# Kernel tuning notes

Measured on AMD Instinct MI355X. Metric: run time of the kernel, lower is better.

The kernel has to match this reference:

```python
import jax, jax.numpy as jnp
import numpy as np

THRESH = 0.7
MIN_KEPT_FRAC = 0.5  # max(0.001, 0.5)
LOG_CLAMP = -100.0   # torch BCELoss clamps log terms at -100


def setup_inputs() -> dict:
    key = jax.random.key(0)
    k1, k2 = jax.random.split(key)
    shape = (32, 1, 1024, 1024)
    pred = jax.random.uniform(k1, shape, dtype=jnp.float32, minval=1e-6, maxval=1.0 - 1e-6)
    target = jnp.round(jax.random.uniform(k2, shape, dtype=jnp.float32))  # binary mask
    return {"pred": pred, "target": target}


def reference(pred, target):
    p = pred.reshape(-1)
    t = target.reshape(-1)
    # elementwise BCE with reduction='none' (torch clamps log at -100)
    log_p = jnp.clip(jnp.log(p), LOG_CLAMP, None)
    log_1mp = jnp.clip(jnp.log1p(-p), LOG_CLAMP, None)
    pixel_losses = -(t * log_p + (1.0 - t) * log_1mp)

    n = p.shape[0]
    min_kept = min(int(MIN_KEPT_FRAC * (n - 1)), n - 1)  # static python int
    p_sorted = jnp.sort(p)
    min_value = p_sorted[min_kept]
    threshold = jnp.maximum(min_value, jnp.float32(THRESH))

    # keeping losses whose pred value is below the threshold; mean over kept
    mask = p < threshold
    cnt = jnp.sum(mask).astype(pixel_losses.dtype)
    return jnp.sum(jnp.where(mask, pixel_losses, 0.0)) / cnt
```

## Files before the change

### kernel.cpp

```cpp
#include <hip/hip_runtime.h>

#define THRESH   0.7f
#define BASEU    0x3F333334u
#define NBINS    2048
#define NSUB     4096
#define NTHREADS 256
#define IPT4     4
#define NITER    4
#define F4_PER_BLOCK (NTHREADS * IPT4 * NITER)
#define MAXBLK   8192
#define NBLK_FB  1024

struct Blk { float sum_lt, sum_eq; unsigned cnt_lt, cnt_eq; };

struct Ws {
  Blk      blk[MAXBLK];
  double   sum_lt, sum_eq;
  double   prefix_sum;
  unsigned cnt_lt, cnt_eq;
  unsigned done;
  unsigned fin3, fin5;
  unsigned selBin, rank_r, prefix_cnt;
  unsigned Hcnt[NBINS];
  float    Hsum[NBINS];
  unsigned subCnt[NSUB];
  float    subSum[NSUB];
};

__device__ __forceinline__ float bce_loss(float p, float t) {
  float x = (t > 0.5f) ? p : (1.0f - p);
  return -fmaxf(__logf(x), -100.0f);
}

__global__ __launch_bounds__(NTHREADS) void k_main(
    const float4* __restrict__ p4, const float4* __restrict__ t4,
    Ws* __restrict__ ws, int n) {
  const int nvec = n >> 2;
  const int start = blockIdx.x * F4_PER_BLOCK;

  float s_lt = 0.f, s_eq = 0.f;
  unsigned c_lt = 0u, c_eq = 0u;

  if (start + F4_PER_BLOCK <= nvec) {
    for (int it = 0; it < NITER; ++it) {
      const int base = start + it * (NTHREADS * IPT4) + threadIdx.x;
      float4 pr[IPT4], tr[IPT4];
#pragma unroll
      for (int j = 0; j < IPT4; ++j) pr[j] = p4[base + j * NTHREADS];
#pragma unroll
      for (int j = 0; j < IPT4; ++j) tr[j] = t4[base + j * NTHREADS];
#pragma unroll
      for (int j = 0; j < IPT4; ++j) {
        float pa[4] = {pr[j].x, pr[j].y, pr[j].z, pr[j].w};
        float ta[4] = {tr[j].x, tr[j].y, tr[j].z, tr[j].w};
#pragma unroll
        for (int c = 0; c < 4; ++c) {
          float pv = pa[c];
          float loss = bce_loss(pv, ta[c]);
          if (pv < THRESH)       { c_lt++; s_lt += loss; }
          else if (pv == THRESH) { c_eq++; s_eq += loss; }
        }
      }
    }
  } else {
    for (int it = 0; it < NITER; ++it) {
      const int base = start + it * (NTHREADS * IPT4) + threadIdx.x;
#pragma unroll
      for (int j = 0; j < IPT4; ++j) {
        int id = base + j * NTHREADS;
        if (id < nvec) {
          float4 p = p4[id];
          float4 t = t4[id];
          float pa[4] = {p.x, p.y, p.z, p.w};
          float ta[4] = {t.x, t.y, t.z, t.w};
#pragma unroll
          for (int c = 0; c < 4; ++c) {
            float pv = pa[c];
            float loss = bce_loss(pv, ta[c]);
            if (pv < THRESH)       { c_lt++; s_lt += loss; }
            else if (pv == THRESH) { c_eq++; s_eq += loss; }
          }
        }
      }
    }
    int i = (nvec << 2) + threadIdx.x;
    if (blockIdx.x == gridDim.x - 1 && i < n) {
      float pv = ((const float*)p4)[i];
      float loss = bce_loss(pv, ((const float*)t4)[i]);
      if (pv < THRESH)       { c_lt++; s_lt += loss; }
      else if (pv == THRESH) { c_eq++; s_eq += loss; }
    }
  }

#pragma unroll
  for (int off = 32; off > 0; off >>= 1) {
    s_lt += __shfl_down(s_lt, off);
    s_eq += __shfl_down(s_eq, off);
    c_lt += __shfl_down(c_lt, off);
    c_eq += __shfl_down(c_eq, off);
  }
  __shared__ float    red_slt[4], red_seq[4];
  __shared__ unsigned red_clt[4], red_ceq[4];
  int wave = threadIdx.x >> 6;
  if ((threadIdx.x & 63) == 0) {
    red_slt[wave] = s_lt; red_seq[wave] = s_eq;
    red_clt[wave] = c_lt; red_ceq[wave] = c_eq;
  }
  __syncthreads();
  if (threadIdx.x == 0) {
    Blk b;
    b.sum_lt = red_slt[0] + red_slt[1] + red_slt[2] + red_slt[3];
    b.sum_eq = red_seq[0] + red_seq[1] + red_seq[2] + red_seq[3];
    b.cnt_lt = red_clt[0] + red_clt[1] + red_clt[2] + red_clt[3];
    b.cnt_eq = red_ceq[0] + red_ceq[1] + red_ceq[2] + red_ceq[3];
    ws->blk[blockIdx.x] = b;
  }
}

__global__ __launch_bounds__(1024) void k_reduce(
    float* __restrict__ out, Ws* __restrict__ ws, int nblk, int kidx) {
  double s_lt = 0.0, s_eq = 0.0;
  unsigned long long c_lt = 0, c_eq = 0;
  for (int i = threadIdx.x; i < nblk; i += 1024) {
    Blk b = ws->blk[i];
    s_lt += (double)b.sum_lt; s_eq += (double)b.sum_eq;
    c_lt += b.cnt_lt;         c_eq += b.cnt_eq;
  }
#pragma unroll
  for (int off = 32; off > 0; off >>= 1) {
    s_lt += __shfl_down(s_lt, off);
    s_eq += __shfl_down(s_eq, off);
    c_lt += __shfl_down(c_lt, off);
    c_eq += __shfl_down(c_eq, off);
  }
  __shared__ double    rs[16], rq[16];
  __shared__ unsigned long long rc[16], re[16];
  int wave = threadIdx.x >> 6;
  if ((threadIdx.x & 63) == 0) { rs[wave] = s_lt; rq[wave] = s_eq; rc[wave] = c_lt; re[wave] = c_eq; }
  __syncthreads();
  if (threadIdx.x == 0) {
    double slt = 0.0, seq = 0.0; unsigned long long clt = 0, ceq = 0;
    for (int w = 0; w < 16; ++w) { slt += rs[w]; seq += rq[w]; clt += rc[w]; ceq += re[w]; }
    ws->sum_lt = slt; ws->sum_eq = seq;
    ws->cnt_lt = (unsigned)clt; ws->cnt_eq = (unsigned)ceq;
    if (clt + ceq > (unsigned long long)kidx) {
      out[0] = (float)(slt / (double)clt);
      ws->done = 1u;
    }
  }
}

__global__ __launch_bounds__(NTHREADS) void k_hist(
    const float* __restrict__ pred, const float* __restrict__ targ,
    Ws* __restrict__ ws, int n, int kidx, int nblocks) {
  if (ws->done) return;
  __shared__ unsigned hc[NBINS];
  __shared__ float    hs[NBINS];
  for (int i = threadIdx.x; i < NBINS; i += NTHREADS) { hc[i] = 0u; hs[i] = 0.f; }
  __syncthreads();

  int tid = blockIdx.x * blockDim.x + threadIdx.x;
  int stride = gridDim.x * blockDim.x;
  int nvec = n >> 2;
  const float4* p4 = (const float4*)pred;
  const float4* t4 = (const float4*)targ;
  for (int i = tid; i < nvec; i += stride) {
    float4 p = p4[i];
    float4 t = t4[i];
    float pa[4] = {p.x, p.y, p.z, p.w};
    float ta[4] = {t.x, t.y, t.z, t.w};
#pragma unroll
    for (int c = 0; c < 4; ++c) {
      float pv = pa[c];
      if (pv > THRESH) {
        unsigned b = (__float_as_uint(pv) - BASEU) >> 12;
        if (b > NBINS - 1) b = NBINS - 1;
        atomicAdd(&hc[b], 1u);
        atomicAdd(&hs[b], bce_loss(pv, ta[c]));
      }
    }
  }
  for (int i = (nvec << 2) + tid; i < n; i += stride) {
    float pv = pred[i];
    if (pv > THRESH) {
      unsigned b = (__float_as_uint(pv) - BASEU) >> 12;
      if (b > NBINS - 1) b = NBINS - 1;
      atomicAdd(&hc[b], 1u);
      atomicAdd(&hs[b], bce_loss(pv, targ[i]));
    }
  }
  __syncthreads();
  for (int i = threadIdx.x; i < NBINS; i += NTHREADS) {
    if (hc[i])        atomicAdd(&ws->Hcnt[i], hc[i]);
    if (hs[i] != 0.f) atomicAdd(&ws->Hsum[i], hs[i]);
  }
  __threadfence();
  if (threadIdx.x == 0) {
    unsigned prev = atomicAdd(&ws->fin3, 1u);
    if (prev == (unsigned)(nblocks - 1)) {
      __threadfence();
      unsigned long long cum  = (unsigned long long)ws->cnt_lt + ws->cnt_eq;
      double             csum = ws->sum_lt + ws->sum_eq;
      for (int b = 0; b < NBINS; ++b) {
        unsigned hcnt = atomicAdd(&ws->Hcnt[b], 0u);
        if (cum + hcnt > (unsigned long long)kidx) {
          ws->selBin     = (unsigned)b;
          ws->rank_r     = (unsigned)((unsigned long long)kidx - cum);
          ws->prefix_cnt = (unsigned)cum;
          ws->prefix_sum = csum;
          break;
        }
        cum  += hcnt;
        csum += (double)atomicAdd(&ws->Hsum[b], 0.f);
      }
    }
  }
}

__global__ __launch_bounds__(NTHREADS) void k_sub(
    const float* __restrict__ pred, const float* __restrict__ targ,
    float* __restrict__ out, Ws* __restrict__ ws, int n, int nblocks) {
  if (ws->done) return;
  unsigned base = BASEU + (ws->selBin << 12);
  __shared__ unsigned sc[NSUB];
  __shared__ float    ssm[NSUB];
  for (int i = threadIdx.x; i < NSUB; i += NTHREADS) { sc[i] = 0u; ssm[i] = 0.f; }
  __syncthreads();

  int tid = blockIdx.x * blockDim.x + threadIdx.x;
  int stride = gridDim.x * blockDim.x;
  int nvec = n >> 2;
  const float4* p4 = (const float4*)pred;
  const float4* t4 = (const float4*)targ;
  for (int i = tid; i < nvec; i += stride) {
    float4 p = p4[i];
    float4 t = t4[i];
    float pa[4] = {p.x, p.y, p.z, p.w};
    float ta[4] = {t.x, t.y, t.z, t.w};
#pragma unroll
    for (int c = 0; c < 4; ++c) {
      unsigned u = __float_as_uint(pa[c]);
      if (u >= base && u < base + NSUB) {
        atomicAdd(&sc[u - base], 1u);
        atomicAdd(&ssm[u - base], bce_loss(pa[c], ta[c]));
      }
    }
  }
  for (int i = (nvec << 2) + tid; i < n; i += stride) {
    unsigned u = __float_as_uint(pred[i]);
    if (u >= base && u < base + NSUB) {
      atomicAdd(&sc[u - base], 1u);
      atomicAdd(&ssm[u - base], bce_loss(pred[i], targ[i]));
    }
  }
  __syncthreads();
  for (int i = threadIdx.x; i < NSUB; i += NTHREADS) {
    if (sc[i])         atomicAdd(&ws->subCnt[i], sc[i]);
    if (ssm[i] != 0.f) atomicAdd(&ws->subSum[i], ssm[i]);
  }
  __threadfence();
  if (threadIdx.x == 0) {
    unsigned prev = atomicAdd(&ws->fin5, 1u);
    if (prev == (unsigned)(nblocks - 1)) {
      __threadfence();
      unsigned r = ws->rank_r;
      unsigned long long cum = 0;
      double csum = 0.0;
      for (int i = 0; i < NSUB; ++i) {
        unsigned c = atomicAdd(&ws->subCnt[i], 0u);
        if (cum + c > (unsigned long long)r) {
          unsigned long long cnt_final = (unsigned long long)ws->prefix_cnt + cum;
          double sum_final = ws->prefix_sum + csum;
          out[0] = (float)(sum_final / (double)cnt_final);
          break;
        }
        cum  += c;
        csum += (double)atomicAdd(&ws->subSum[i], 0.f);
      }
    }
  }
}

extern "C" void kernel_launch(void* const* d_in, const int* in_sizes, int n_in,
                              void* d_out, int out_size, void* d_ws, size_t ws_size,
                              hipStream_t stream) {
  const float* pred = (const float*)d_in[0];
  const float* targ = (const float*)d_in[1];
  float* out = (float*)d_out;
  Ws* ws = (Ws*)d_ws;
  int n = in_sizes[0];
  long long kll = (long long)(n - 1) / 2;
  if (kll > (long long)(n - 1)) kll = n - 1;
  int kidx = (int)kll;

  int nvec = n >> 2;
  int nblk = (nvec + F4_PER_BLOCK - 1) / F4_PER_BLOCK;
  if (nblk < 1) nblk = 1;
  if (nblk > MAXBLK) nblk = MAXBLK;

  hipMemsetAsync(d_ws, 0, sizeof(Ws), stream);
  k_main  <<<nblk, NTHREADS, 0, stream>>>((const float4*)pred, (const float4*)targ, ws, n);
  k_reduce<<<1, 1024, 0, stream>>>(out, ws, nblk, kidx);
  k_hist  <<<NBLK_FB, NTHREADS, 0, stream>>>(pred, targ, ws, n, kidx, NBLK_FB);
  k_sub   <<<NBLK_FB, NTHREADS, 0, stream>>>(pred, targ, out, ws, n, NBLK_FB);
}
```

Baseline: 290.7 us.

## Drop workspace memset, merge fallback kernels with grid sync, software-pipeline main loads

Removes the full-workspace hipMemsetAsync and resets counters inside the decide kernel instead. The two fallback histogram kernels become one kernel that clears its own arrays and uses spin-based grid barriers. The main pass gains a grid-stride chunk loop with double-buffered float4 loads, branchless lt accumulation with a wave-level __any guard for the equality case, and launch bounds requesting 4 blocks per CU. This cuts launch and memset overhead and improves memory-level parallelism, but the spin barrier risks deadlock if all 1024 fallback blocks are not co-resident.

```diff
diff --git a/kernel.cpp b/kernel.cpp
--- a/kernel.cpp
+++ b/kernel.cpp
@@ -5,9 +5,7 @@
 #define NBINS    2048
 #define NSUB     4096
 #define NTHREADS 256
-#define IPT4     4
-#define NITER    4
-#define F4_PER_BLOCK (NTHREADS * IPT4 * NITER)
+#define F4_PER_CHUNK 4096
 #define MAXBLK   8192
 #define NBLK_FB  1024
 
@@ -15,11 +13,10 @@
 
 struct Ws {
   Blk      blk[MAXBLK];
-  double   sum_lt, sum_eq;
-  double   prefix_sum;
+  double   sum_lt, sum_eq, prefix_sum;
   unsigned cnt_lt, cnt_eq;
   unsigned done;
-  unsigned fin3, fin5;
+  unsigned fin0, fin1, fin2, fin3;
   unsigned selBin, rank_r, prefix_cnt;
   unsigned Hcnt[NBINS];
   float    Hsum[NBINS];
@@ -29,66 +26,80 @@
 
 __device__ __forceinline__ float bce_loss(float p, float t) {
   float x = (t > 0.5f) ? p : (1.0f - p);
-  return -fmaxf(__logf(x), -100.0f);
-}
-
-__global__ __launch_bounds__(NTHREADS) void k_main(
+  return fminf(-__logf(x), 100.0f);
+}
+
+__global__ __launch_bounds__(NTHREADS, 4) void k_main(
     const float4* __restrict__ p4, const float4* __restrict__ t4,
-    Ws* __restrict__ ws, int n) {
+    Ws* __restrict__ ws, int n, int nchunks) {
   const int nvec = n >> 2;
-  const int start = blockIdx.x * F4_PER_BLOCK;
-
   float s_lt = 0.f, s_eq = 0.f;
   unsigned c_lt = 0u, c_eq = 0u;
 
-  if (start + F4_PER_BLOCK <= nvec) {
-    for (int it = 0; it < NITER; ++it) {
-      const int base = start + it * (NTHREADS * IPT4) + threadIdx.x;
-      float4 pr[IPT4], tr[IPT4];
-#pragma unroll
-      for (int j = 0; j < IPT4; ++j) pr[j] = p4[base + j * NTHREADS];
-#pragma unroll
-      for (int j = 0; j < IPT4; ++j) tr[j] = t4[base + j * NTHREADS];
-#pragma unroll
-      for (int j = 0; j < IPT4; ++j) {
-        float pa[4] = {pr[j].x, pr[j].y, pr[j].z, pr[j].w};
-        float ta[4] = {tr[j].x, tr[j].y, tr[j].z, tr[j].w};
+#define CONSUME(PR, TR)                                                        \
+  _Pragma("unroll") for (int j = 0; j < 4; ++j) {                              \
+    float pa[4] = {PR[j].x, PR[j].y, PR[j].z, PR[j].w};                        \
+    float ta[4] = {TR[j].x, TR[j].y, TR[j].z, TR[j].w};                        \
+    _Pragma("unroll") for (int c = 0; c < 4; ++c) {                            \
+      float pv = pa[c];                                                        \
+      float x  = (ta[c] > 0.5f) ? pv : (1.0f - pv);                            \
+      float l  = fminf(-__logf(x), 100.0f);                                    \
+      bool lt  = (pv < THRESH);                                                \
+      s_lt += lt ? l : 0.0f;                                                   \
+      c_lt += lt ? 1u : 0u;                                                    \
+      if (__any(pv == THRESH)) {               \
+        bool eq = (pv == THRESH);                                              \
+        c_eq += eq ? 1u : 0u;                                                  \
+        s_eq += eq ? l : 0.0f;                                                 \
+      }                                                                        \
+    }                                                                          \
+  }
+#define LOADB(PR, TR, IT)                                                      \
+  _Pragma("unroll") for (int j = 0; j < 4; ++j) {                              \
+    PR[j] = pp[(IT) * 1024 + j * 256];                                         \
+    TR[j] = tt[(IT) * 1024 + j * 256];                                         \
+  }
+
+  for (int chunk = blockIdx.x; chunk < nchunks; chunk += gridDim.x) {
+    const int start = chunk * F4_PER_CHUNK;
+    if (start + F4_PER_CHUNK <= nvec) {
+      const float4* pp = p4 + start + threadIdx.x;
+      const float4* tt = t4 + start + threadIdx.x;
+      float4 pA[4], tA[4], pB[4], tB[4];
+      LOADB(pA, tA, 0)
+      LOADB(pB, tB, 1)
+      CONSUME(pA, tA)
+      LOADB(pA, tA, 2)
+      CONSUME(pB, tB)
+      LOADB(pB, tB, 3)
+      CONSUME(pA, tA)
+      CONSUME(pB, tB)
+    } else {
+      int lim = start + F4_PER_CHUNK; if (lim > nvec) lim = nvec;
+      for (int f = start + threadIdx.x; f < lim; f += NTHREADS) {
+        float4 p = p4[f];
+        float4 t = t4[f];
+        float pa[4] = {p.x, p.y, p.z, p.w};
+        float ta[4] = {t.x, t.y, t.z, t.w};
 #pragma unroll
         for (int c = 0; c < 4; ++c) {
           float pv = pa[c];
-          float loss = bce_loss(pv, ta[c]);
-          if (pv < THRESH)       { c_lt++; s_lt += loss; }
-          else if (pv == THRESH) { c_eq++; s_eq += loss; }
+          float l = bce_loss(pv, ta[c]);
+          if (pv < THRESH)       { c_lt++; s_lt += l; }
+          else if (pv == THRESH) { c_eq++; s_eq += l; }
         }
       }
     }
-  } else {
-    for (int it = 0; it < NITER; ++it) {
-      const int base = start + it * (NTHREADS * IPT4) + threadIdx.x;
-#pragma unroll
-      for (int j = 0; j < IPT4; ++j) {
-        int id = base + j * NTHREADS;
-        if (id < nvec) {
-          float4 p = p4[id];
-          float4 t = t4[id];
-          float pa[4] = {p.x, p.y, p.z, p.w};
-          float ta[4] = {t.x, t.y, t.z, t.w};
-#pragma unroll
-          for (int c = 0; c < 4; ++c) {
-            float pv = pa[c];
-            float loss = bce_loss(pv, ta[c]);
-            if (pv < THRESH)       { c_lt++; s_lt += loss; }
-            else if (pv == THRESH) { c_eq++; s_eq += loss; }
-          }
-        }
-      }
-    }
+  }
+#undef LOADB
+#undef CONSUME
+  if (blockIdx.x == 0) {
     int i = (nvec << 2) + threadIdx.x;
-    if (blockIdx.x == gridDim.x - 1 && i < n) {
+    if (i < n) {
       float pv = ((const float*)p4)[i];
-      float loss = bce_loss(pv, ((const float*)t4)[i]);
-      if (pv < THRESH)       { c_lt++; s_lt += loss; }
-      else if (pv == THRESH) { c_eq++; s_eq += loss; }
+      float l = bce_loss(pv, ((const float*)t4)[i]);
+      if (pv < THRESH)       { c_lt++; s_lt += l; }
+      else if (pv == THRESH) { c_eq++; s_eq += l; }
     }
   }
 
@@ -117,7 +128,7 @@
   }
 }
 
-__global__ __launch_bounds__(1024) void k_reduce(
+__global__ __launch_bounds__(1024) void k_decide(
     float* __restrict__ out, Ws* __restrict__ ws, int nblk, int kidx) {
   double s_lt = 0.0, s_eq = 0.0;
   unsigned long long c_lt = 0, c_eq = 0;
@@ -133,7 +144,7 @@
     c_lt += __shfl_down(c_lt, off);
     c_eq += __shfl_down(c_eq, off);
   }
-  __shared__ double    rs[16], rq[16];
+  __shared__ double rs[16], rq[16];
   __shared__ unsigned long long rc[16], re[16];
   int wave = threadIdx.x >> 6;
   if ((threadIdx.x & 63) == 0) { rs[wave] = s_lt; rq[wave] = s_eq; rc[wave] = c_lt; re[wave] = c_eq; }
@@ -143,140 +154,111 @@
     for (int w = 0; w < 16; ++w) { slt += rs[w]; seq += rq[w]; clt += rc[w]; ceq += re[w]; }
     ws->sum_lt = slt; ws->sum_eq = seq;
     ws->cnt_lt = (unsigned)clt; ws->cnt_eq = (unsigned)ceq;
+    ws->fin0 = 0u; ws->fin1 = 0u; ws->fin2 = 0u; ws->fin3 = 0u;
     if (clt + ceq > (unsigned long long)kidx) {
       out[0] = (float)(slt / (double)clt);
       ws->done = 1u;
-    }
-  }
-}
-
-__global__ __launch_bounds__(NTHREADS) void k_hist(
+    } else {
+      ws->done = 0u;
+    }
+  }
+}
+
+__device__ void gsync(unsigned* ctr, unsigned goal) {
+  __syncthreads();
+  if (threadIdx.x == 0) {
+    __threadfence();
+    atomicAdd(ctr, 1u);
+    while (atomicAdd(ctr, 0u) < goal) __builtin_amdgcn_s_sleep(8);
+  }
+  __syncthreads();
+  __threadfence();
+}
+
+__global__ __launch_bounds__(NTHREADS) void k_fallback(
     const float* __restrict__ pred, const float* __restrict__ targ,
-    Ws* __restrict__ ws, int n, int kidx, int nblocks) {
+    float* __restrict__ out, Ws* __restrict__ ws, int n, int kidx) {
   if (ws->done) return;
-  __shared__ unsigned hc[NBINS];
-  __shared__ float    hs[NBINS];
-  for (int i = threadIdx.x; i < NBINS; i += NTHREADS) { hc[i] = 0u; hs[i] = 0.f; }
-  __syncthreads();
-
-  int tid = blockIdx.x * blockDim.x + threadIdx.x;
-  int stride = gridDim.x * blockDim.x;
-  int nvec = n >> 2;
-  const float4* p4 = (const float4*)pred;
-  const float4* t4 = (const float4*)targ;
-  for (int i = tid; i < nvec; i += stride) {
-    float4 p = p4[i];
-    float4 t = t4[i];
-    float pa[4] = {p.x, p.y, p.z, p.w};
-    float ta[4] = {t.x, t.y, t.z, t.w};
-#pragma unroll
-    for (int c = 0; c < 4; ++c) {
-      float pv = pa[c];
-      if (pv > THRESH) {
-        unsigned b = (__float_as_uint(pv) - BASEU) >> 12;
-        if (b > NBINS - 1) b = NBINS - 1;
-        atomicAdd(&hc[b], 1u);
-        atomicAdd(&hs[b], bce_loss(pv, ta[c]));
-      }
-    }
-  }
-  for (int i = (nvec << 2) + tid; i < n; i += stride) {
+
+  __shared__ union {
+    struct { unsigned hc[NBINS]; float hs[NBINS]; } l1;
+    struct { unsigned sc[NSUB];  float ss[NSUB];  } l2;
+  } sh;
+
+  const int gtid = blockIdx.x * NTHREADS + threadIdx.x;
+  const int gstride = gridDim.x * NTHREADS;
+
+  for (int i = gtid; i < NBINS; i += gstride) { ws->Hcnt[i] = 0u; ws->Hsum[i] = 0.f; }
+  for (int i = gtid; i < NSUB;  i += gstride) { ws->subCnt[i] = 0u; ws->subSum[i] = 0.f; }
+  gsync(&ws->fin0, gridDim.x);
+
+  for (int i = threadIdx.x; i < NBINS; i += NTHREADS) { sh.l1.hc[i] = 0u; sh.l1.hs[i] = 0.f; }
+  __syncthreads();
+  for (int i = gtid; i < n; i += gstride) {
     float pv = pred[i];
     if (pv > THRESH) {
       unsigned b = (__float_as_uint(pv) - BASEU) >> 12;
       if (b > NBINS - 1) b = NBINS - 1;
-      atomicAdd(&hc[b], 1u);
-      atomicAdd(&hs[b], bce_loss(pv, targ[i]));
+      atomicAdd(&sh.l1.hc[b], 1u);
+      atomicAdd(&sh.l1.hs[b], bce_loss(pv, targ[i]));
     }
   }
   __syncthreads();
   for (int i = threadIdx.x; i < NBINS; i += NTHREADS) {
-    if (hc[i])        atomicAdd(&ws->Hcnt[i], hc[i]);
-    if (hs[i] != 0.f) atomicAdd(&ws->Hsum[i], hs[i]);
-  }
-  __threadfence();
-  if (threadIdx.x == 0) {
-    unsigned prev = atomicAdd(&ws->fin3, 1u);
-    if (prev == (unsigned)(nblocks - 1)) {
-      __threadfence();
-      unsigned long long cum  = (unsigned long long)ws->cnt_lt + ws->cnt_eq;
-      double             csum = ws->sum_lt + ws->sum_eq;
-      for (int b = 0; b < NBINS; ++b) {
-        unsigned hcnt = atomicAdd(&ws->Hcnt[b], 0u);
-        if (cum + hcnt > (unsigned long long)kidx) {
-          ws->selBin     = (unsigned)b;
-          ws->rank_r     = (unsigned)((unsigned long long)kidx - cum);
-          ws->prefix_cnt = (unsigned)cum;
-          ws->prefix_sum = csum;
-          break;
-        }
-        cum  += hcnt;
-        csum += (double)atomicAdd(&ws->Hsum[b], 0.f);
+    if (sh.l1.hc[i])        atomicAdd(&ws->Hcnt[i], sh.l1.hc[i]);
+    if (sh.l1.hs[i] != 0.f) atomicAdd(&ws->Hsum[i], sh.l1.hs[i]);
+  }
+  gsync(&ws->fin1, gridDim.x);
+
+  if (blockIdx.x == 0 && threadIdx.x == 0) {
+    unsigned long long cum = (unsigned long long)ws->cnt_lt + ws->cnt_eq;
+    double csum = ws->sum_lt + ws->sum_eq;
+    for (int b = 0; b < NBINS; ++b) {
+      unsigned hcnt = atomicAdd(&ws->Hcnt[b], 0u);
+      if (cum + hcnt > (unsigned long long)kidx) {
+        atomicExch(&ws->selBin, (unsigned)b);
+        atomicExch(&ws->rank_r, (unsigned)((unsigned long long)kidx - cum));
+        atomicExch(&ws->prefix_cnt, (unsigned)cum);
+        ws->prefix_sum = csum;
+        break;
       }
-    }
-  }
-}
-
-__global__ __launch_bounds__(NTHREADS) void k_sub(
-    const float* __restrict__ pred, const float* __restrict__ targ,
-    float* __restrict__ out, Ws* __restrict__ ws, int n, int nblocks) {
-  if (ws->done) return;
-  unsigned base = BASEU + (ws->selBin << 12);
-  __shared__ unsigned sc[NSUB];
-  __shared__ float    ssm[NSUB];
-  for (int i = threadIdx.x; i < NSUB; i += NTHREADS) { sc[i] = 0u; ssm[i] = 0.f; }
-  __syncthreads();
-
-  int tid = blockIdx.x * blockDim.x + threadIdx.x;
-  int stride = gridDim.x * blockDim.x;
-  int nvec = n >> 2;
-  const float4* p4 = (const float4*)pred;
-  const float4* t4 = (const float4*)targ;
-  for (int i = tid; i < nvec; i += stride) {
-    float4 p = p4[i];
-    float4 t = t4[i];
-    float pa[4] = {p.x, p.y, p.z, p.w};
-    float ta[4] = {t.x, t.y, t.z, t.w};
-#pragma unroll
-    for (int c = 0; c < 4; ++c) {
-      unsigned u = __float_as_uint(pa[c]);
-      if (u >= base && u < base + NSUB) {
-        atomicAdd(&sc[u - base], 1u);
-        atomicAdd(&ssm[u - base], bce_loss(pa[c], ta[c]));
-      }
-    }
-  }
-  for (int i = (nvec << 2) + tid; i < n; i += stride) {
+      cum  += hcnt;
+      csum += (double)atomicAdd(&ws->Hsum[b], 0.f);
+    }
+  }
+  gsync(&ws->fin2, gridDim.x);
+
+  unsigned base = BASEU + (atomicAdd(&ws->selBin, 0u) << 12);
+  for (int i = threadIdx.x; i < NSUB; i += NTHREADS) { sh.l2.sc[i] = 0u; sh.l2.ss[i] = 0.f; }
+  __syncthreads();
+  for (int i = gtid; i < n; i += gstride) {
     unsigned u = __float_as_uint(pred[i]);
     if (u >= base && u < base + NSUB) {
-      atomicAdd(&sc[u - base], 1u);
-      atomicAdd(&ssm[u - base], bce_loss(pred[i], targ[i]));
+      atomicAdd(&sh.l2.sc[u - base], 1u);
+      atomicAdd(&sh.l2.ss[u - base], bce_loss(pred[i], targ[i]));
     }
   }
   __syncthreads();
   for (int i = threadIdx.x; i < NSUB; i += NTHREADS) {
-    if (sc[i])         atomicAdd(&ws->subCnt[i], sc[i]);
-    if (ssm[i] != 0.f) atomicAdd(&ws->subSum[i], ssm[i]);
-  }
-  __threadfence();
-  if (threadIdx.x == 0) {
-    unsigned prev = atomicAdd(&ws->fin5, 1u);
-    if (prev == (unsigned)(nblocks - 1)) {
-      __threadfence();
-      unsigned r = ws->rank_r;
-      unsigned long long cum = 0;
-      double csum = 0.0;
-      for (int i = 0; i < NSUB; ++i) {
-        unsigned c = atomicAdd(&ws->subCnt[i], 0u);
-        if (cum + c > (unsigned long long)r) {
-          unsigned long long cnt_final = (unsigned long long)ws->prefix_cnt + cum;
-          double sum_final = ws->prefix_sum + csum;
-          out[0] = (float)(sum_final / (double)cnt_final);
-          break;
-        }
-        cum  += c;
-        csum += (double)atomicAdd(&ws->subSum[i], 0.f);
+    if (sh.l2.sc[i])         atomicAdd(&ws->subCnt[i], sh.l2.sc[i]);
+    if (sh.l2.ss[i] != 0.f)  atomicAdd(&ws->subSum[i], sh.l2.ss[i]);
+  }
+  gsync(&ws->fin3, gridDim.x);
+
+  if (blockIdx.x == 0 && threadIdx.x == 0) {
+    unsigned r = atomicAdd(&ws->rank_r, 0u);
+    unsigned long long cum = 0;
+    double csum = 0.0;
+    for (int i = 0; i < NSUB; ++i) {
+      unsigned c = atomicAdd(&ws->subCnt[i], 0u);
+      if (cum + c > (unsigned long long)r) {
+        unsigned long long cnt_final = (unsigned long long)atomicAdd(&ws->prefix_cnt, 0u) + cum;
+        double sum_final = ws->prefix_sum + csum;
+        out[0] = (float)(sum_final / (double)cnt_final);
+        break;
       }
+      cum  += c;
+      csum += (double)atomicAdd(&ws->subSum[i], 0.f);
     }
   }
 }
@@ -294,13 +276,11 @@
   int kidx = (int)kll;
 
   int nvec = n >> 2;
-  int nblk = (nvec + F4_PER_BLOCK - 1) / F4_PER_BLOCK;
-  if (nblk < 1) nblk = 1;
-  if (nblk > MAXBLK) nblk = MAXBLK;
-
-  hipMemsetAsync(d_ws, 0, sizeof(Ws), stream);
-  k_main  <<<nblk, NTHREADS, 0, stream>>>((const float4*)pred, (const float4*)targ, ws, n);
-  k_reduce<<<1, 1024, 0, stream>>>(out, ws, nblk, kidx);
-  k_hist  <<<NBLK_FB, NTHREADS, 0, stream>>>(pred, targ, ws, n, kidx, NBLK_FB);
-  k_sub   <<<NBLK_FB, NTHREADS, 0, stream>>>(pred, targ, out, ws, n, NBLK_FB);
-}
+  int nchunks = (nvec + F4_PER_CHUNK - 1) / F4_PER_CHUNK;
+  if (nchunks < 1) nchunks = 1;
+  int nblk = nchunks > MAXBLK ? MAXBLK : nchunks;
+
+  k_main    <<<nblk, NTHREADS, 0, stream>>>((const float4*)pred, (const float4*)targ, ws, n, nchunks);
+  k_decide  <<<1, 1024, 0, stream>>>(out, ws, nblk, kidx);
+  k_fallback<<<NBLK_FB, NTHREADS, 0, stream>>>(pred, targ, out, ws, n, kidx);
+}
```

After: 283.2 us. 2.6% less time.
